# Kernel optimization log

Hardware: AMD Instinct MI355X
Metric: run time of the kernel (lower is better)

The kernel has to match this reference:

```python
import jax, jax.numpy as jnp
import numpy as np


def setup_inputs() -> dict:
    key = jax.random.key(0)
    k1, k2, k3 = jax.random.split(key, 3)
    B, C_in, C_out, T = 16, 512, 512, 4096
    pre = jax.random.normal(k1, (B, C_in, T), dtype=jnp.float32)
    # nn.Linear weight layout: [out_features, in_features]
    W_pre = jax.random.normal(k2, (C_out, C_in), dtype=jnp.float32) * (1.0 / np.sqrt(C_in))
    b_pre = jax.random.normal(k3, (C_out,), dtype=jnp.float32) * 0.01
    return {"pre": pre, "W_pre": W_pre, "b_pre": b_pre}


def reference(pre, W_pre, b_pre):
    # Original 'casual' branch loops over T applying w_pre(_pre[:,:,i]) into BOTH
    # embedding_prev and embedding_curr, then sums -> 2 * (W_pre @ pre + b).
    # Batched form: one einsum over the full sequence.
    y = jnp.einsum('bct,oc->bot', pre, W_pre) + b_pre[None, :, None]  # [B, C_out, T]
    return y + y
```

## Files before the change

kernel.cpp:

```cpp
#include <hip/hip_runtime.h>
#include <hip/hip_bf16.h>

typedef __attribute__((ext_vector_type(8))) short short8_t;
typedef __attribute__((ext_vector_type(4))) float f32x4;

#define BATCH 16
#define CIN   512
#define COUT  512
#define TT    4096
#define BKT   32
#define NKT   16

__device__ __forceinline__ uint pk2(float a, float b) {
    ushort lo = __builtin_bit_cast(ushort, __float2bfloat16(a));
    ushort hi = __builtin_bit_cast(ushort, __float2bfloat16(b));
    return (uint)lo | ((uint)hi << 16);
}

#define SCHEDB()   __builtin_amdgcn_sched_barrier(0)
#define WAIT_VM(N) do { asm volatile("s_waitcnt vmcnt(" #N ")" ::: "memory"); SCHEDB(); } while (0)
#define WAIT_LGKM() do { asm volatile("s_waitcnt lgkmcnt(0)" ::: "memory"); SCHEDB(); } while (0)
#define RAW_BARRIER() do { __builtin_amdgcn_s_barrier(); SCHEDB(); } while (0)

extern "C" __global__ __launch_bounds__(256)
void wconv(const float* __restrict__ W, ushort* __restrict__ Wb)
{
    const int i  = blockIdx.x * 256 + threadIdx.x;
    const int m  = i >> 7;
    const int k0 = (i & 127) * 4;
    const float4 v = *(const float4*)(W + (size_t)m * CIN + k0);
    const int bm = m >> 4, r = m & 15;
    const int ksg = k0 >> 5, g = (k0 >> 3) & 3, k7 = k0 & 7;
    uint2 q;
    q.x = pk2(v.x, v.y);
    q.y = pk2(v.z, v.w);
    *(uint2*)&Wb[(size_t)bm * 8192 + ksg * 512 + g * 128 + r * 8 + k7] = q;
}

template<bool WSB>
__global__ __launch_bounds__(256)
void conv2x1_gemm(const float* __restrict__ pre, const float* __restrict__ W,
                  const ushort* __restrict__ Wb,
                  const float* __restrict__ bias, float* __restrict__ out)
{
    __shared__ float  RAW[3][BKT * 64];
    __shared__ ushort BF [2][4 * 64 * 8];

    const int tid  = threadIdx.x;
    const int lane = tid & 63;
    const int wv   = tid >> 6;
    const int g    = lane >> 4;
    const int l15  = lane & 15;

    const int id   = ((blockIdx.x & 7) << 9) | (blockIdx.x >> 3);
    const int mblk = id & 3;
    const int ti   = (id >> 2) & 63;
    const int bb   = id >> 8;

    const int m0 = mblk << 7;
    const int t0 = ti << 6;

    const float* preB   = pre + (size_t)bb * ((size_t)CIN * TT);
    const int    bmBase = (m0 >> 4) + wv * 2;

    f32x4 acc[2][4];
#pragma unroll
    for (int i = 0; i < 2; ++i)
#pragma unroll
        for (int j = 0; j < 4; ++j) acc[i][j] = (f32x4)0.0f;

#define STAGE(J) do { \
    _Pragma("unroll") \
    for (int i = 0; i < 2; ++i) { \
        const int krow = wv*8 + i*4 + (lane >> 4); \
        const float* gsrc = preB + (size_t)((J)*BKT + krow) * TT + t0 + ((lane & 15) << 2); \
        float* ldst = &RAW[(J) % 3][(wv*128 + i*64 + lane) * 4]; \
        __builtin_amdgcn_global_load_lds((const __attribute__((address_space(1))) void*)gsrc, \
                                         (__attribute__((address_space(3))) void*)ldst, 16, 0, 0); \
    } } while (0)

#define LOAD_A(KT, AF) do { \
    if constexpr (WSB) { \
        _Pragma("unroll") \
        for (int mi = 0; mi < 2; ++mi) \
            AF[mi] = *(const short8_t*)(Wb + (size_t)(bmBase + mi) * 8192 \
                                        + (KT) * 512 + g * 128 + l15 * 8); \
    } else { \
        _Pragma("unroll") \
        for (int mi = 0; mi < 2; ++mi) { \
            const float* ab = W + (size_t)(m0 + wv*32 + mi*16 + l15) * CIN + (KT)*BKT + g*8; \
            const float4 u0 = *(const float4*)ab; \
            const float4 u1 = *(const float4*)(ab + 4); \
            uint4 qq; \
            qq.x = pk2(u0.x, u0.y); qq.y = pk2(u0.z, u0.w); \
            qq.z = pk2(u1.x, u1.y); qq.w = pk2(u1.z, u1.w); \
            AF[mi] = __builtin_bit_cast(short8_t, qq); \
        } \
    } } while (0)

#define CVT(J) do { \
    const int ct = tid & 63; \
    float f[8]; \
    _Pragma("unroll") \
    for (int j = 0; j < 8; ++j) \
        f[j] = RAW[(J) % 3][(wv*8 + j) * 64 + ct]; \
    uint4 q; \
    q.x = pk2(f[0], f[1]); \
    q.y = pk2(f[2], f[3]); \
    q.z = pk2(f[4], f[5]); \
    q.w = pk2(f[6], f[7]); \
    *(uint4*)&BF[(J) & 1][wv * 512 + ct * 8] = q; \
    } while (0)

#define MFMA_STEP(J, AF) do { \
    short8_t bf[4]; \
    _Pragma("unroll") \
    for (int ni = 0; ni < 4; ++ni) \
        bf[ni] = *(const short8_t*)&BF[(J) & 1][g * 512 + (ni*16 + l15) * 8]; \
    _Pragma("unroll") \
    for (int mi = 0; mi < 2; ++mi) \
        _Pragma("unroll") \
        for (int ni = 0; ni < 4; ++ni) \
            acc[mi][ni] = __builtin_amdgcn_mfma_f32_16x16x32_bf16(AF[mi], bf[ni], acc[mi][ni], 0, 0, 0); \
    } while (0)

    STAGE(0);
    STAGE(1);
    WAIT_VM(2);
    RAW_BARRIER();
    CVT(0);

#pragma unroll
    for (int kt = 0; kt < NKT; ++kt) {
        short8_t af[2];
        LOAD_A(kt, af);
        if (kt + 2 < NKT) {
            STAGE(kt + 2);
            WAIT_VM(2);
        } else {
            WAIT_VM(0);
        }
        WAIT_LGKM();
        RAW_BARRIER();
        MFMA_STEP(kt, af);
        if (kt + 1 < NKT) CVT(kt + 1);
    }

    const int orow = m0 + wv*32 + g*4;
    float bv[2][4];
#pragma unroll
    for (int mi = 0; mi < 2; ++mi)
#pragma unroll
        for (int r = 0; r < 4; ++r)
            bv[mi][r] = bias[orow + mi*16 + r];

    float* outB = out + (size_t)bb * ((size_t)COUT * TT);
#pragma unroll
    for (int mi = 0; mi < 2; ++mi) {
#pragma unroll
        for (int ni = 0; ni < 4; ++ni) {
            const int t = t0 + ni*16 + l15;
#pragma unroll
            for (int r = 0; r < 4; ++r) {
                const int o = orow + mi*16 + r;
                outB[(size_t)o * TT + t] = 2.0f * (acc[mi][ni][r] + bv[mi][r]);
            }
        }
    }
}

extern "C" void kernel_launch(void* const* d_in, const int* in_sizes, int n_in,
                              void* d_out, int out_size, void* d_ws, size_t ws_size,
                              hipStream_t stream)
{
    const float* pre  = (const float*)d_in[0];
    const float* Wp   = (const float*)d_in[1];
    const float* bias = (const float*)d_in[2];
    float* out = (float*)d_out;

    const size_t wb_bytes = (size_t)COUT * CIN * sizeof(ushort);

    const dim3 grid(BATCH * 4 * 64);
    const dim3 block(256);

    if (ws_size >= wb_bytes) {
        ushort* Wb = (ushort*)d_ws;
        hipLaunchKernelGGL(wconv, dim3(256), dim3(256), 0, stream, Wp, Wb);
        hipLaunchKernelGGL((conv2x1_gemm<true>), grid, block, 0, stream,
                           pre, Wp, Wb, bias, out);
    } else {
        hipLaunchKernelGGL((conv2x1_gemm<false>), grid, block, 0, stream,
                           pre, Wp, (const ushort*)nullptr, bias, out);
    }
}
```

Baseline: 81.72 us.

## Make GEMM blocks persistent over T chunks with register-resident weight fragments

Grid shrinks to 512 blocks, and each block walks 8 consecutive 64-wide T tiles. The block's whole 128x512 bf16 weight slice is held in registers (af[16][2]) and loaded once, instead of reloading A fragments every k-step. The K step doubles to 64, with a 3-deep raw LDS pipeline spanning tiles, split convert read/write around the MFMAs, and setprio raised around the MFMA issue. The cost is heavy VGPR pressure, which may lower occupancy or cause spills, and fewer blocks for load balancing.

```diff
diff --git a/kernel.cpp b/kernel.cpp
--- a/kernel.cpp
+++ b/kernel.cpp
@@ -8,8 +8,8 @@
 #define CIN   512
 #define COUT  512
 #define TT    4096
-#define BKT   32
-#define NKT   16
+#define BKT   64
+#define NS    64
 
 __device__ __forceinline__ uint pk2(float a, float b) {
     ushort lo = __builtin_bit_cast(ushort, __float2bfloat16(a));
@@ -17,8 +17,10 @@
     return (uint)lo | ((uint)hi << 16);
 }
 
-#define SCHEDB()   __builtin_amdgcn_sched_barrier(0)
-#define WAIT_VM(N) do { asm volatile("s_waitcnt vmcnt(" #N ")" ::: "memory"); SCHEDB(); } while (0)
+#define SCHEDB()    __builtin_amdgcn_sched_barrier(0)
+#define WAIT_VM4()  do { asm volatile("s_waitcnt vmcnt(4)" ::: "memory"); SCHEDB(); } while (0)
+#define WAIT_VM0()  do { asm volatile("s_waitcnt vmcnt(0)" ::: "memory"); SCHEDB(); } while (0)
+#define WAIT_VM8()  do { asm volatile("s_waitcnt vmcnt(8)" ::: "memory"); SCHEDB(); } while (0)
 #define WAIT_LGKM() do { asm volatile("s_waitcnt lgkmcnt(0)" ::: "memory"); SCHEDB(); } while (0)
 #define RAW_BARRIER() do { __builtin_amdgcn_s_barrier(); SCHEDB(); } while (0)
 
@@ -44,7 +46,7 @@
                   const float* __restrict__ bias, float* __restrict__ out)
 {
     __shared__ float  RAW[3][BKT * 64];
-    __shared__ ushort BF [2][4 * 64 * 8];
+    __shared__ ushort BF [2][8 * 64 * 8];
 
     const int tid  = threadIdx.x;
     const int lane = tid & 63;
@@ -52,118 +54,138 @@
     const int g    = lane >> 4;
     const int l15  = lane & 15;
 
-    const int id   = ((blockIdx.x & 7) << 9) | (blockIdx.x >> 3);
-    const int mblk = id & 3;
-    const int ti   = (id >> 2) & 63;
-    const int bb   = id >> 8;
-
-    const int m0 = mblk << 7;
-    const int t0 = ti << 6;
-
-    const float* preB   = pre + (size_t)bb * ((size_t)CIN * TT);
-    const int    bmBase = (m0 >> 4) + wv * 2;
-
-    f32x4 acc[2][4];
-#pragma unroll
-    for (int i = 0; i < 2; ++i)
-#pragma unroll
-        for (int j = 0; j < 4; ++j) acc[i][j] = (f32x4)0.0f;
-
-#define STAGE(J) do { \
-    _Pragma("unroll") \
-    for (int i = 0; i < 2; ++i) { \
-        const int krow = wv*8 + i*4 + (lane >> 4); \
-        const float* gsrc = preB + (size_t)((J)*BKT + krow) * TT + t0 + ((lane & 15) << 2); \
-        float* ldst = &RAW[(J) % 3][(wv*128 + i*64 + lane) * 4]; \
+    const int id     = ((blockIdx.x & 7) << 6) | (blockIdx.x >> 3);
+    const int mstrip = id & 3;
+    const int tch    = (id >> 2) & 7;
+    const int bb     = id >> 5;
+
+    const int m0    = mstrip << 7;
+    const int tbase = tch << 9;
+
+    const float* preB = pre + (size_t)bb * ((size_t)CIN * TT);
+    const int bmBase  = (m0 >> 4) + wv * 2;
+
+    short8_t af[16][2];
+    if constexpr (WSB) {
+#pragma unroll
+        for (int ksg = 0; ksg < 16; ++ksg)
+#pragma unroll
+            for (int mi = 0; mi < 2; ++mi)
+                af[ksg][mi] = *(const short8_t*)(Wb + (size_t)(bmBase + mi) * 8192
+                                                 + ksg * 512 + g * 128 + l15 * 8);
+    } else {
+#pragma unroll
+        for (int ksg = 0; ksg < 16; ++ksg)
+#pragma unroll
+            for (int mi = 0; mi < 2; ++mi) {
+                const float* ab = W + (size_t)(m0 + wv*32 + mi*16 + l15) * CIN + ksg*32 + g*8;
+                const float4 u0 = *(const float4*)ab;
+                const float4 u1 = *(const float4*)(ab + 4);
+                uint4 qq;
+                qq.x = pk2(u0.x, u0.y); qq.y = pk2(u0.z, u0.w);
+                qq.z = pk2(u1.x, u1.y); qq.w = pk2(u1.z, u1.w);
+                af[ksg][mi] = __builtin_bit_cast(short8_t, qq);
+            }
+    }
+
+    float bv[2][4];
+#pragma unroll
+    for (int mi = 0; mi < 2; ++mi)
+#pragma unroll
+        for (int r = 0; r < 4; ++r)
+            bv[mi][r] = bias[m0 + wv*32 + g*4 + mi*16 + r];
+
+    float f[16];
+
+#define STAGE(S) do { \
+    const int kc = ((S) & 7) * BKT; \
+    const int tc = tbase + (((S) >> 3) << 6); \
+    _Pragma("unroll") \
+    for (int i = 0; i < 4; ++i) { \
+        const int krow = wv*16 + i*4 + (lane >> 4); \
+        const float* gsrc = preB + (size_t)(kc + krow) * TT + tc + ((lane & 15) << 2); \
+        float* ldst = &RAW[(S) % 3][(wv*16 + i*4)*64 + lane*4]; \
         __builtin_amdgcn_global_load_lds((const __attribute__((address_space(1))) void*)gsrc, \
                                          (__attribute__((address_space(3))) void*)ldst, 16, 0, 0); \
     } } while (0)
 
-#define LOAD_A(KT, AF) do { \
-    if constexpr (WSB) { \
+#define CVT_READ(S) do { \
+    const int ct = tid & 63; \
+    _Pragma("unroll") \
+    for (int j = 0; j < 16; ++j) \
+        f[j] = RAW[(S) % 3][(wv*16 + j) * 64 + ct]; \
+    } while (0)
+
+#define CVT_WRITE(S) do { \
+    const int ct = tid & 63; \
+    _Pragma("unroll") \
+    for (int h = 0; h < 2; ++h) { \
+        uint4 q; \
+        q.x = pk2(f[h*8+0], f[h*8+1]); \
+        q.y = pk2(f[h*8+2], f[h*8+3]); \
+        q.z = pk2(f[h*8+4], f[h*8+5]); \
+        q.w = pk2(f[h*8+6], f[h*8+7]); \
+        *(uint4*)&BF[(S) & 1][(wv*2 + h) * 512 + ct * 8] = q; \
+    } } while (0)
+
+#define MFMA_STEP(S, KT) do { \
+    __builtin_amdgcn_s_setprio(1); \
+    _Pragma("unroll") \
+    for (int ks = 0; ks < 2; ++ks) { \
+        short8_t bf[4]; \
+        _Pragma("unroll") \
+        for (int ni = 0; ni < 4; ++ni) \
+            bf[ni] = *(const short8_t*)&BF[(S) & 1][(ks*4 + g) * 512 + (ni*16 + l15) * 8]; \
         _Pragma("unroll") \
         for (int mi = 0; mi < 2; ++mi) \
-            AF[mi] = *(const short8_t*)(Wb + (size_t)(bmBase + mi) * 8192 \
-                                        + (KT) * 512 + g * 128 + l15 * 8); \
-    } else { \
-        _Pragma("unroll") \
-        for (int mi = 0; mi < 2; ++mi) { \
-            const float* ab = W + (size_t)(m0 + wv*32 + mi*16 + l15) * CIN + (KT)*BKT + g*8; \
-            const float4 u0 = *(const float4*)ab; \
-            const float4 u1 = *(const float4*)(ab + 4); \
-            uint4 qq; \
-            qq.x = pk2(u0.x, u0.y); qq.y = pk2(u0.z, u0.w); \
-            qq.z = pk2(u1.x, u1.y); qq.w = pk2(u1.z, u1.w); \
-            AF[mi] = __builtin_bit_cast(short8_t, qq); \
-        } \
-    } } while (0)
-
-#define CVT(J) do { \
-    const int ct = tid & 63; \
-    float f[8]; \
-    _Pragma("unroll") \
-    for (int j = 0; j < 8; ++j) \
-        f[j] = RAW[(J) % 3][(wv*8 + j) * 64 + ct]; \
-    uint4 q; \
-    q.x = pk2(f[0], f[1]); \
-    q.y = pk2(f[2], f[3]); \
-    q.z = pk2(f[4], f[5]); \
-    q.w = pk2(f[6], f[7]); \
-    *(uint4*)&BF[(J) & 1][wv * 512 + ct * 8] = q; \
+            _Pragma("unroll") \
+            for (int ni = 0; ni < 4; ++ni) \
+                acc[mi][ni] = __builtin_amdgcn_mfma_f32_16x16x32_bf16(af[(KT)*2+ks][mi], bf[ni], acc[mi][ni], 0, 0, 0); \
+    } \
+    __builtin_amdgcn_s_setprio(0); \
     } while (0)
 
-#define MFMA_STEP(J, AF) do { \
-    short8_t bf[4]; \
-    _Pragma("unroll") \
-    for (int ni = 0; ni < 4; ++ni) \
-        bf[ni] = *(const short8_t*)&BF[(J) & 1][g * 512 + (ni*16 + l15) * 8]; \
-    _Pragma("unroll") \
-    for (int mi = 0; mi < 2; ++mi) \
-        _Pragma("unroll") \
-        for (int ni = 0; ni < 4; ++ni) \
-            acc[mi][ni] = __builtin_amdgcn_mfma_f32_16x16x32_bf16(AF[mi], bf[ni], acc[mi][ni], 0, 0, 0); \
-    } while (0)
-
-    STAGE(0);
-    STAGE(1);
-    WAIT_VM(2);
+    STAGE(0); STAGE(1); STAGE(2);
+    WAIT_VM8();
     RAW_BARRIER();
-    CVT(0);
-
-#pragma unroll
-    for (int kt = 0; kt < NKT; ++kt) {
-        short8_t af[2];
-        LOAD_A(kt, af);
-        if (kt + 2 < NKT) {
-            STAGE(kt + 2);
-            WAIT_VM(2);
-        } else {
-            WAIT_VM(0);
+    CVT_READ(0);
+    CVT_WRITE(0);
+
+    f32x4 acc[2][4];
+#pragma unroll
+    for (int i = 0; i < 2; ++i)
+#pragma unroll
+        for (int j = 0; j < 4; ++j) acc[i][j] = (f32x4)0.0f;
+
+    float* outB = out + (size_t)bb * ((size_t)COUT * TT);
+
+    for (int tt = 0; tt < 8; ++tt) {
+#pragma unroll
+        for (int kt = 0; kt < 8; ++kt) {
+            const int s = tt * 8 + kt;
+            if (s + 2 < NS) WAIT_VM4();
+            else            WAIT_VM0();
+            WAIT_LGKM();
+            RAW_BARRIER();
+            if (s + 3 < NS) STAGE(s + 3);
+            if (s + 1 < NS) CVT_READ(s + 1);
+            MFMA_STEP(s, kt);
+            if (s + 1 < NS) CVT_WRITE(s + 1);
         }
-        WAIT_LGKM();
-        RAW_BARRIER();
-        MFMA_STEP(kt, af);
-        if (kt + 1 < NKT) CVT(kt + 1);
-    }
-
-    const int orow = m0 + wv*32 + g*4;
-    float bv[2][4];
-#pragma unroll
-    for (int mi = 0; mi < 2; ++mi)
-#pragma unroll
-        for (int r = 0; r < 4; ++r)
-            bv[mi][r] = bias[orow + mi*16 + r];
-
-    float* outB = out + (size_t)bb * ((size_t)COUT * TT);
-#pragma unroll
-    for (int mi = 0; mi < 2; ++mi) {
-#pragma unroll
-        for (int ni = 0; ni < 4; ++ni) {
-            const int t = t0 + ni*16 + l15;
-#pragma unroll
-            for (int r = 0; r < 4; ++r) {
-                const int o = orow + mi*16 + r;
-                outB[(size_t)o * TT + t] = 2.0f * (acc[mi][ni][r] + bv[mi][r]);
+
+        const int orow = m0 + wv*32 + g*4;
+        const int tcol = tbase + tt*64;
+#pragma unroll
+        for (int mi = 0; mi < 2; ++mi) {
+#pragma unroll
+            for (int ni = 0; ni < 4; ++ni) {
+                const int t = tcol + ni*16 + l15;
+#pragma unroll
+                for (int r = 0; r < 4; ++r) {
+                    const int o = orow + mi*16 + r;
+                    outB[(size_t)o * TT + t] = 2.0f * (acc[mi][ni][r] + bv[mi][r]);
+                }
+                acc[mi][ni] = (f32x4)0.0f;
             }
         }
     }
@@ -180,7 +202,7 @@
 
     const size_t wb_bytes = (size_t)COUT * CIN * sizeof(ushort);
 
-    const dim3 grid(BATCH * 4 * 64);
+    const dim3 grid(512);
     const dim3 block(256);
 
     if (ws_size >= wb_bytes) {
```

Measured after the change: 114.5 us. 1.4x slower.
